# Performance work log

Measured on AMD Instinct MI355X. Metric: run time of the kernel, lower is better.

The kernel has to match this reference:

```python
import jax, jax.numpy as jnp
import numpy as np

jax.config.update("jax_enable_x64", True)  # original solves the quartic in double/complex128

MU = 1.33
SCALE = 1.0
N_RAYS = 2_000_000


def _solve2nd(a, b, c):
    # roots of a x^2 + b x + c, complex128
    D = (b * b - 4 * a * c).astype(jnp.complex128)
    s = jnp.sqrt(D)
    return (-b + s) / (2 * a), (-b - s) / (2 * a)


def _solve3rd(a, b, c, d):
    # Cardano closed form, returns [N,3] complex128
    A0 = d / a
    A1 = c / a
    A2 = b / a
    p = A1 - A2 * A2 / 3
    q = A0 - A1 * A2 / 3 + A2 * A2 * A2 * 2 / 27
    D = (q / 2) ** 2 + (p / 3) ** 3 + 1e-12
    r = jnp.sqrt(D.astype(jnp.complex128))
    o = complex(-0.5, np.sqrt(3) / 2)
    L = jnp.power(-q / 2 + r, 1.0 / 3.0)
    R = jnp.power(-q / 2 - r, 1.0 / 3.0)
    x0 = L + R - A2 / 3
    x1 = o * o * L + o * R - A2 / 3
    x2 = o * L + o * o * R - A2 / 3
    return jnp.stack([x0, x1, x2], axis=-1)


def _solve4th(coefs):
    # Ferrari via resolvent cubic; coefs [N,5] float64 -> roots [N,4] complex128
    a, b, c, d, e = (coefs[..., i] for i in range(5))
    A0 = e / a
    A1 = d / a
    A2 = c / a
    A3 = b / a
    p = A2 - 6 * A3 * A3 / 16
    q = A1 - A2 * A3 / 2 + 8 * (A3 / 4) ** 3
    r = A0 - A1 * A3 / 4 + A2 * A3 * A3 / 16 - 3 * (A3 / 4) ** 4
    u = _solve3rd(jnp.ones_like(p), 2 * p, p * p - 4 * r, -q * q)  # [N,3] complex
    cost = jnp.where(u.real < 0, 1e6, jnp.abs(u.imag))
    idx = jnp.argmin(cost, axis=1)
    t = jnp.clip(jnp.take_along_axis(u.real, idx[:, None], axis=1)[:, 0], 1e-6, None)
    st = jnp.sqrt(t)
    y00, y01 = _solve2nd(jnp.ones_like(t), st, (p + t) / 2 - st * q / (2 * t))
    y10, y11 = _solve2nd(jnp.ones_like(t), -st, (p + t) / 2 + st * q / (2 * t))
    return jnp.stack([y00 - A3 / 4, y01 - A3 / 4, y10 - A3 / 4, y11 - A3 / 4], axis=-1)


def _forward_projection(pos3d, n, d_eff, mu):
    nvec = jnp.concatenate([n, jnp.ones((1,), pos3d.dtype)])
    normal = -(nvec / jnp.linalg.norm(nvec))[None, :]          # [1,3]
    por = jnp.cross(normal, pos3d)                              # [N,3]
    por = por / jnp.linalg.norm(por, axis=-1, keepdims=True)
    z1 = -normal                                                # [1,3]
    z2 = jnp.cross(por, jnp.broadcast_to(z1, por.shape))        # [N,3]
    v = jnp.sum(pos3d * z1, axis=-1)                            # [N]
    u = jnp.sum(pos3d * z2, axis=-1)                            # [N]
    c2 = -2 * u * (mu - 1) * (mu + 1)
    c1 = jnp.ones_like(c2) * ((mu - 1) * (mu + 1))
    c3 = d_eff * d_eff * mu * mu - d_eff * d_eff + 2 * d_eff * v + mu * mu * u * u - u * u - v * v
    c4 = -2 * d_eff * d_eff * mu * mu * u
    c5 = d_eff * d_eff * mu * mu * u * u
    coefs = jnp.stack([c1, c2, c3, c4, c5], axis=-1).astype(jnp.float64)
    x0 = _solve4th(coefs).astype(jnp.complex64).T               # [4,N]
    xx = x0.real.astype(jnp.float32)                            # [4,N]
    n2 = jnp.array([0.0, -1.0], jnp.float32)
    vi = jnp.stack([xx, jnp.ones_like(xx) * d_eff], axis=-1)    # [4,N,2]
    bb = jnp.sum(vi * n2, axis=-1)
    bbb = jnp.sum(vi * vi, axis=-1)
    b = (-bb - jnp.sqrt(bb * bb - (1 - mu * mu) * bbb)) / mu
    vr = (1.0 / mu) * vi + b[..., None] * n2                    # refracted 2D dirs
    vrd = jnp.stack([u, v], axis=-1)[None] - vi                 # [4,N,2]
    error = jnp.abs(vrd[..., 0] * vr[..., 1] - vrd[..., 1] * vr[..., 0])
    error = jnp.where(jnp.abs(x0.imag) > 0.001, jnp.inf, error)
    best = jnp.take_along_axis(xx, jnp.argmin(error, axis=0)[None, :], axis=0)[0]
    return best[:, None] * z2 + d_eff * z1                      # [N,3]


def setup_inputs() -> dict:
    key = jax.random.key(0)
    k1, k2, k3 = jax.random.split(key, 3)
    pos3d = jax.random.normal(k1, (N_RAYS, 3), dtype=jnp.float32)
    # put points at positive depth so refraction geometry is sensible
    pos3d = pos3d.at[:, 2].set(jnp.abs(pos3d[:, 2]) + 0.5)
    n = jax.random.normal(k2, (2,), dtype=jnp.float32) * 0.02   # near-flat interface normal xy
    d = jax.random.uniform(k3, (), dtype=jnp.float32) * 0.5 + 0.2  # scalar depth param
    return {"pos3d": pos3d, "n": n, "d": d}


def reference(pos3d, n, d):
    mu = jnp.float32(MU)
    d_eff = jax.nn.relu(d) / SCALE + 0.001
    return _forward_projection(pos3d, n, d_eff, mu)
```

## Files before the change

kernel.cpp:

```cpp
#include <hip/hip_runtime.h>
#include <math.h>


__device__ __forceinline__ float fast_rcp(float x) { return __builtin_amdgcn_rcpf(x); }
__device__ __forceinline__ float fast_rsq(float x) { return __builtin_amdgcn_rsqf(x); }

__device__ __forceinline__ void cbrt_cw(double x, double& c, double& w) {
    float xf = (float)x;
    float wf = __builtin_amdgcn_exp2f(__builtin_amdgcn_logf(xf) * (-1.0f / 3.0f));
    double wd = (double)wf;
    wd = wd * (4.0 - x * ((wd * wd) * wd)) * (1.0 / 3.0);
    bool tiny = (x < 1e-30);
    w = tiny ? 0.0 : wd;
    c = tiny ? 0.0 : x * (wd * wd);
}

__global__ __launch_bounds__(256) void refract_kernel(
    const float* __restrict__ pos,
    const float* __restrict__ nrm,
    const float* __restrict__ dpt,
    float* __restrict__ out,
    int N)
{
    int i = blockIdx.x * blockDim.x + threadIdx.x;
    if (i >= N) return;

    const float mu = 1.33f;
    float n0 = nrm[0], n1 = nrm[1];
    float d_eff = fmaxf(dpt[0], 0.0f) + 0.001f;

    float nn = sqrtf(n0 * n0 + n1 * n1 + 1.0f);
    float z1x = n0 / nn, z1y = n1 / nn, z1z = 1.0f / nn;

    float px = pos[3 * i + 0], py = pos[3 * i + 1], pz = pos[3 * i + 2];

    float cux = z1y * pz - z1z * py;
    float cuy = z1z * px - z1x * pz;
    float cuz = z1x * py - z1y * px;
    float pn = sqrtf(cux * cux + cuy * cuy + cuz * cuz);
    float u = -pn;
    float ipn = fast_rcp(pn);
    float z2x = (z1y * cuz - z1z * cuy) * ipn;
    float z2y = (z1z * cux - z1x * cuz) * ipn;
    float z2z = (z1x * cuy - z1y * cux) * ipn;

    float v = px * z1x + py * z1y + pz * z1z;

    float c3f = d_eff * d_eff * mu * mu - d_eff * d_eff + 2.0f * d_eff * v
              + mu * mu * u * u - u * u - v * v;

    const double invc1 = 1.0 / (double)((1.33f - 1.0f) * (1.33f + 1.0f));
    const double mu2d = (double)(1.33f) * (double)(1.33f);
    double dm = (double)d_eff;
    double km = -2.0 * dm * dm * mu2d * invc1;

    double ud = (double)u;
    double G  = (double)c3f * invc1;
    double U  = ud * ud;
    double p  = fma(-1.5, U, G);
    double q  = ud * ((G - U) + km);
    double r  = 0.25 * U * fma(-0.75, U, G);
    double p2 = p * p;
    double q2 = q * q;
    double pr = p * r;
    double p3 = p2 * p;
    double mql = fma(p3, 1.0 / 27.0, fma(pr, -4.0 / 3.0, 0.5 * q2));
    double pc3 = fma(p2, -1.0 / 9.0, (-4.0 / 3.0) * r);
    double Dc  = fma(pc3 * pc3, pc3, fma(mql, mql, 1e-12));
    double sh  = p * (2.0 / 3.0);
    double p2d = p + p;

    double t;

    if (Dc < 0.0) {
        float R2f = (float)(-pc3);
        float Rf  = sqrtf(R2f);
        float cphi = (float)mql * fast_rcp(R2f * Rf);
        cphi = fminf(fmaxf(cphi, -1.0f), 1.0f);
        float T = 0.5f + sqrtf((1.0f + cphi) * (1.0f / 6.0f));
        #pragma unroll
        for (int k = 0; k < 3; ++k) {
            float g  = fmaf(fmaf(4.0f * T, T, -3.0f), T, -cphi);
            float gp = fmaf(12.0f * T, T, -3.0f);
            T -= g * fast_rcp(gp + 1e-12f);
        }
        t = (double)(2.0f * Rf * T) - sh;

        double B1n = fma(-4.0, r, p2);
        double f   = ((t + p2d) * t + B1n) * t - q2;
        double fp  = fma(3.0 * t + p2d, t, (t * p2d + B1n));
        double fpp = 6.0 * t + 2.0 * p2d;
        double den = fp * fp - 0.5 * f * fpp;
        double inv = (double)fast_rcp((float)den);
        inv = inv * (2.0 - den * inv);
        double dt  = (f * fp) * inv;
        if (isfinite(dt) && fabs(dt) < 0.1 * fabs(t) + 1e-2) t -= dt;
    } else {
        double rcr;
        if (Dc < 1e-36) {
            rcr = 0.0;
        } else {
            double z = (double)fast_rsq((float)Dc);
            z = z * (1.5 - 0.5 * Dc * (z * z));
            rcr = Dc * z;
        }
        double aa = mql + rcr;
        double bb = mql - rcr;
        bool na = (aa < 0.0), nb = (bb < 0.0);

        double absa = fabs(aa), absb = fabs(bb);
        bool aBig = (absa >= absb);
        double big = aBig ? absa : absb;
        double cbig, wbig;
        cbrt_cw(big, cbig, wbig);
        double csml = fabs(pc3) * wbig;
        double ca = aBig ? cbig : csml;
        double cb = aBig ? csml : cbig;

        if (!na && !nb) {
            double s = ca + cb;
            double u0r = s - sh;
            t = (u0r >= 0.0) ? u0r : fma(-0.5, s, -sh);
        } else {
            const double CI = 0.8660254037844386;
            double Lre = na ? 0.5 * ca : ca;
            double Lim = na ? CI * ca  : 0.0;
            double Rre = nb ? 0.5 * cb : cb;
            double Rim = nb ? CI * cb  : 0.0;

            double u0r = (Lre + Rre) - sh;
            double u0i =  Lim + Rim;
            double u1r = (-0.5 * Lre + CI * Lim) + (-0.5 * Rre - CI * Rim) - sh;
            double u1i = (-0.5 * Lim - CI * Lre) + (-0.5 * Rim + CI * Rre);
            double u2r = (-0.5 * Lre - CI * Lim) + (-0.5 * Rre + CI * Rim) - sh;
            double u2i = (-0.5 * Lim + CI * Lre) + (-0.5 * Rim - CI * Rre);

            double c0 = (u0r < 0.0) ? 1e6 : fabs(u0i);
            double c1 = (u1r < 0.0) ? 1e6 : fabs(u1i);
            double c2 = (u2r < 0.0) ? 1e6 : fabs(u2i);
            double cbest = c0; t = u0r;
            if (c1 < cbest) { cbest = c1; t = u1r; }
            if (c2 < cbest) { t = u2r; }
        }
    }

    t = fmax(t, 1e-6);
    double rs = (double)fast_rsq((float)t);
    rs = rs * (1.5 - 0.5 * t * (rs * rs));
    double st = t * rs;
    double tp = t + p2d;
    double wq = 2.0 * (q * rs);
    double D1 = wq - tp;
    double D2 = -wq - tp;

    float s1r = 0.0f, s1i = 0.0f, s2r = 0.0f, s2i = 0.0f;
    if (D1 >= 0.0) s1r = sqrtf((float)D1); else s1i = sqrtf((float)(-D1));
    if (D2 >= 0.0) s2r = sqrtf((float)D2); else s2i = sqrtf((float)(-D2));
    bool im1 = (s1i * 0.5f > 0.001f);
    bool im2 = (s2i * 0.5f > 0.001f);

    float stf = (float)st;
    float uh  = 0.5f * u;
    float xr0 = (-stf + s1r) * 0.5f + uh;
    float xr1 = (-stf - s1r) * 0.5f + uh;
    float xr2 = ( stf + s2r) * 0.5f + uh;
    float xr3 = ( stf - s2r) * 0.5f + uh;

    float mm2 = mu * mu - 1.0f;
    float mude2 = mu * mu * d_eff * d_eff;
    float vd = v - d_eff;
    float g0 = fmaf(mm2, xr0 * xr0, mude2);
    float g1 = fmaf(mm2, xr1 * xr1, mude2);
    float g2 = fmaf(mm2, xr2 * xr2, mude2);
    float g3 = fmaf(mm2, xr3 * xr3, mude2);
    float e0 = im1 ? INFINITY : fabsf((u - xr0) * sqrtf(g0) - vd * xr0);
    float e1 = im1 ? INFINITY : fabsf((u - xr1) * sqrtf(g1) - vd * xr1);
    float e2 = im2 ? INFINITY : fabsf((u - xr2) * sqrtf(g2) - vd * xr2);
    float e3 = im2 ? INFINITY : fabsf((u - xr3) * sqrtf(g3) - vd * xr3);

    float best = xr0; float eb = e0;
    if (e1 < eb) { eb = e1; best = xr1; }
    if (e2 < eb) { eb = e2; best = xr2; }
    if (e3 < eb) { eb = e3; best = xr3; }

    out[3 * i + 0] = best * z2x + d_eff * z1x;
    out[3 * i + 1] = best * z2y + d_eff * z1y;
    out[3 * i + 2] = best * z2z + d_eff * z1z;
}

extern "C" void kernel_launch(void* const* d_in, const int* in_sizes, int n_in,
                              void* d_out, int out_size, void* d_ws, size_t ws_size,
                              hipStream_t stream) {
    const float* pos = (const float*)d_in[0];
    const float* nrm = (const float*)d_in[1];
    const float* dpt = (const float*)d_in[2];
    float* out = (float*)d_out;
    int N = in_sizes[0] / 3;
    int block = 256;
    int grid = (N + block - 1) / block;
    refract_kernel<<<grid, block, 0, stream>>>(pos, nrm, dpt, out, N);
}
```

Before: 29.00 us.

## Run cubic root branch in fp32 with flagged fp64 rescue path

The non-trigonometric Cardano branch now runs in single precision, using an fp32 cube root and fp32 complex root selection, instead of double precision. A set of conditioning checks marks lanes where fp32 may pick the wrong root: near-zero discriminants, near-tied selection costs, and near-zero quadratic discriminants. Those lanes recompute the full original fp64 path in a noinline rescue function. This aims to cut the slow fp64 work per ray, at the cost of extra flag arithmetic, a divergent rescue call and possible accuracy misses the heuristics do not catch.

New measurement: 40.16 us. +38.5%, slower.

```diff
diff --git a/kernel.cpp b/kernel.cpp
--- a/kernel.cpp
+++ b/kernel.cpp
@@ -5,7 +5,14 @@
 __device__ __forceinline__ float fast_rcp(float x) { return __builtin_amdgcn_rcpf(x); }
 __device__ __forceinline__ float fast_rsq(float x) { return __builtin_amdgcn_rsqf(x); }
 
-__device__ __forceinline__ void cbrt_cw(double x, double& c, double& w) {
+__device__ __forceinline__ float cbrtf_pos(float x) {
+    float w = __builtin_amdgcn_exp2f(__builtin_amdgcn_logf(x) * (-1.0f / 3.0f));
+    w = w * (4.0f - x * ((w * w) * w)) * (1.0f / 3.0f);
+    float c = x * (w * w);
+    return (x < 1e-30f) ? 0.0f : c;
+}
+
+__device__ __forceinline__ void cbrt_cw64(double x, double& c, double& w) {
     float xf = (float)x;
     float wf = __builtin_amdgcn_exp2f(__builtin_amdgcn_logf(xf) * (-1.0f / 3.0f));
     double wd = (double)wf;
@@ -13,6 +20,113 @@
     bool tiny = (x < 1e-30);
     w = tiny ? 0.0 : wd;
     c = tiny ? 0.0 : x * (wd * wd);
+}
+
+__device__ __attribute__((noinline)) float rescue_fp64(
+    double q, double q2, double B1n, double mql, double pc3,
+    double Dc, double sh, double p2d,
+    float u, float mm2, float mude2, float vd)
+{
+    double t;
+    if (Dc < 0.0) {
+        float R2f = (float)(-pc3);
+        float Rf  = sqrtf(R2f);
+        float cphi = (float)mql * fast_rcp(R2f * Rf);
+        cphi = fminf(fmaxf(cphi, -1.0f), 1.0f);
+        float T = 0.5f + sqrtf((1.0f + cphi) * (1.0f / 6.0f));
+        #pragma unroll
+        for (int k = 0; k < 3; ++k) {
+            float g  = fmaf(fmaf(4.0f * T, T, -3.0f), T, -cphi);
+            float gp = fmaf(12.0f * T, T, -3.0f);
+            T -= g * fast_rcp(gp + 1e-12f);
+        }
+        t = (double)(2.0f * Rf * T) - sh;
+        double f   = ((t + p2d) * t + B1n) * t - q2;
+        double fp_ = fma(3.0 * t + p2d, t, (t * p2d + B1n));
+        double fpp = 6.0 * t + 2.0 * p2d;
+        double den = fp_ * fp_ - 0.5 * f * fpp;
+        double inv = (double)fast_rcp((float)den);
+        inv = inv * (2.0 - den * inv);
+        double dt  = (f * fp_) * inv;
+        if (isfinite(dt) && fabs(dt) < 0.1 * fabs(t) + 1e-2) t -= dt;
+    } else {
+        double rcr;
+        if (Dc < 1e-36) rcr = 0.0;
+        else {
+            double z = (double)fast_rsq((float)Dc);
+            z = z * (1.5 - 0.5 * Dc * (z * z));
+            rcr = Dc * z;
+        }
+        double aa = mql + rcr, bb = mql - rcr;
+        bool na = (aa < 0.0), nb = (bb < 0.0);
+        double absa = fabs(aa), absb = fabs(bb);
+        bool aBig = (absa >= absb);
+        double big = aBig ? absa : absb;
+        double cbig, wbig;
+        cbrt_cw64(big, cbig, wbig);
+        double csml = fabs(pc3) * wbig;
+        double ca = aBig ? cbig : csml;
+        double cb = aBig ? csml : cbig;
+        if (!na && !nb) {
+            double s = ca + cb;
+            double u0r = s - sh;
+            t = (u0r >= 0.0) ? u0r : fma(-0.5, s, -sh);
+        } else {
+            const double CI = 0.8660254037844386;
+            double Lre = na ? 0.5 * ca : ca;
+            double Lim = na ? CI * ca  : 0.0;
+            double Rre = nb ? 0.5 * cb : cb;
+            double Rim = nb ? CI * cb  : 0.0;
+            double u0r = (Lre + Rre) - sh;
+            double u0i =  Lim + Rim;
+            double u1r = (-0.5 * Lre + CI * Lim) + (-0.5 * Rre - CI * Rim) - sh;
+            double u1i = (-0.5 * Lim - CI * Lre) + (-0.5 * Rim + CI * Rre);
+            double u2r = (-0.5 * Lre - CI * Lim) + (-0.5 * Rre + CI * Rim) - sh;
+            double u2i = (-0.5 * Lim + CI * Lre) + (-0.5 * Rim - CI * Rre);
+            double c0 = (u0r < 0.0) ? 1e6 : fabs(u0i);
+            double c1 = (u1r < 0.0) ? 1e6 : fabs(u1i);
+            double c2 = (u2r < 0.0) ? 1e6 : fabs(u2i);
+            double cbest = c0; t = u0r;
+            if (c1 < cbest) { cbest = c1; t = u1r; }
+            if (c2 < cbest) { t = u2r; }
+        }
+    }
+
+    t = fmax(t, 1e-6);
+    double rs = (double)fast_rsq((float)t);
+    rs = rs * (1.5 - 0.5 * t * (rs * rs));
+    double wq = 2.0 * (q * rs);
+    double tp = t + p2d;
+    double D1 = wq - tp;
+    double D2 = -wq - tp;
+
+    float s1r = 0.0f, s1i = 0.0f, s2r = 0.0f, s2i = 0.0f;
+    if (D1 >= 0.0) s1r = sqrtf((float)D1); else s1i = sqrtf((float)(-D1));
+    if (D2 >= 0.0) s2r = sqrtf((float)D2); else s2i = sqrtf((float)(-D2));
+    bool im1 = (s1i * 0.5f > 0.001f);
+    bool im2 = (s2i * 0.5f > 0.001f);
+
+    float stf = (float)(t * rs);
+    float uh  = 0.5f * u;
+    float xr0 = (-stf + s1r) * 0.5f + uh;
+    float xr1 = (-stf - s1r) * 0.5f + uh;
+    float xr2 = ( stf + s2r) * 0.5f + uh;
+    float xr3 = ( stf - s2r) * 0.5f + uh;
+
+    float g0 = fmaf(mm2, xr0 * xr0, mude2);
+    float g1 = fmaf(mm2, xr1 * xr1, mude2);
+    float g2 = fmaf(mm2, xr2 * xr2, mude2);
+    float g3 = fmaf(mm2, xr3 * xr3, mude2);
+    float e0 = im1 ? INFINITY : fabsf((u - xr0) * sqrtf(g0) - vd * xr0);
+    float e1 = im1 ? INFINITY : fabsf((u - xr1) * sqrtf(g1) - vd * xr1);
+    float e2 = im2 ? INFINITY : fabsf((u - xr2) * sqrtf(g2) - vd * xr2);
+    float e3 = im2 ? INFINITY : fabsf((u - xr3) * sqrtf(g3) - vd * xr3);
+
+    float best = xr0; float eb = e0;
+    if (e1 < eb) { eb = e1; best = xr1; }
+    if (e2 < eb) { eb = e2; best = xr2; }
+    if (e3 < eb) { eb = e3; best = xr3; }
+    return best;
 }
 
 __global__ __launch_bounds__(256) void refract_kernel(
@@ -66,16 +180,26 @@
     double p3 = p2 * p;
     double mql = fma(p3, 1.0 / 27.0, fma(pr, -4.0 / 3.0, 0.5 * q2));
     double pc3 = fma(p2, -1.0 / 9.0, (-4.0 / 3.0) * r);
-    double Dc  = fma(pc3 * pc3, pc3, fma(mql, mql, 1e-12));
+    double pc33 = (pc3 * pc3) * pc3;
+    double mql2 = mql * mql;
+    double Dc   = pc33 + (mql2 + 1e-12);
+    double scDc = fabs(pc33) + mql2 + 1e-12;
     double sh  = p * (2.0 / 3.0);
     double p2d = p + p;
+    double B1n = fma(-4.0, r, p2);
+
+    bool flag = fabs(Dc) < 1e-12 * scDc;
+
+    float mqlf = (float)mql;
+    float shf  = (float)sh;
 
     double t;
+    bool polish = false;
 
     if (Dc < 0.0) {
         float R2f = (float)(-pc3);
         float Rf  = sqrtf(R2f);
-        float cphi = (float)mql * fast_rcp(R2f * Rf);
+        float cphi = mqlf * fast_rcp(R2f * Rf);
         cphi = fminf(fmaxf(cphi, -1.0f), 1.0f);
         float T = 0.5f + sqrtf((1.0f + cphi) * (1.0f / 6.0f));
         #pragma unroll
@@ -85,81 +209,87 @@
             T -= g * fast_rcp(gp + 1e-12f);
         }
         t = (double)(2.0f * Rf * T) - sh;
-
-        double B1n = fma(-4.0, r, p2);
+        polish = true;
+    } else {
+        float rcrf = sqrtf((float)Dc);
+        float aaf = mqlf + rcrf;
+        float bbf = mqlf - rcrf;
+        float abscale = fabsf(mqlf) + rcrf + 1e-20f;
+        flag = flag || (fabsf(aaf) < 2e-5f * abscale)
+                    || (fabsf(bbf) < 2e-5f * abscale);
+        bool na = (aaf < 0.0f), nb = (bbf < 0.0f);
+        float caf = cbrtf_pos(fabsf(aaf));
+        float cbf = cbrtf_pos(fabsf(bbf));
+
+        if (!na && !nb) {
+            float s = caf + cbf;
+            float u0rf = s - shf;
+            flag = flag || (fabsf(u0rf) < 3e-6f * (s + fabsf(shf) + 1e-20f));
+            if (u0rf >= 0.0f) { t = (double)u0rf; polish = true; }
+            else              { t = (double)fmaf(-0.5f, s, -shf); }
+        } else {
+            const float CI = 0.8660254f;
+            float Lre = na ? 0.5f * caf : caf;
+            float Lim = na ? CI * caf   : 0.0f;
+            float Rre = nb ? 0.5f * cbf : cbf;
+            float Rim = nb ? CI * cbf   : 0.0f;
+            float u0r = (Lre + Rre) - shf;
+            float u0i =  Lim + Rim;
+            float u1r = (-0.5f * Lre + CI * Lim) + (-0.5f * Rre - CI * Rim) - shf;
+            float u1i = (-0.5f * Lim - CI * Lre) + (-0.5f * Rim + CI * Rre);
+            float u2r = (-0.5f * Lre - CI * Lim) + (-0.5f * Rre + CI * Rim) - shf;
+            float u2i = (-0.5f * Lim + CI * Lre) + (-0.5f * Rim - CI * Rre);
+
+            float jscale = caf + cbf + fabsf(shf) + 1e-20f;
+            flag = flag || (fabsf(u0r) < 1e-5f * jscale)
+                        || (fabsf(u1r) < 1e-5f * jscale)
+                        || (fabsf(u2r) < 1e-5f * jscale);
+
+            float c0 = (u0r < 0.0f) ? 1e6f : fabsf(u0i);
+            float c1 = (u1r < 0.0f) ? 1e6f : fabsf(u1i);
+            float c2 = (u2r < 0.0f) ? 1e6f : fabsf(u2i);
+            float cbest = c0, tsel = u0r, csec;
+            if (c1 < cbest) { csec = cbest; cbest = c1; tsel = u1r; }
+            else            { csec = c1; }
+            if (c2 < cbest) { csec = cbest; cbest = c2; tsel = u2r; }
+            else            { csec = fminf(csec, c2); }
+            flag = flag || ((csec - cbest) < 1e-4f * (cbest + 1e-3f));
+            t = (double)tsel;
+        }
+    }
+
+    if (polish) {
         double f   = ((t + p2d) * t + B1n) * t - q2;
-        double fp  = fma(3.0 * t + p2d, t, (t * p2d + B1n));
+        double fp_ = fma(3.0 * t + p2d, t, (t * p2d + B1n));
         double fpp = 6.0 * t + 2.0 * p2d;
-        double den = fp * fp - 0.5 * f * fpp;
+        double den = fp_ * fp_ - 0.5 * f * fpp;
         double inv = (double)fast_rcp((float)den);
         inv = inv * (2.0 - den * inv);
-        double dt  = (f * fp) * inv;
+        double dt  = (f * fp_) * inv;
         if (isfinite(dt) && fabs(dt) < 0.1 * fabs(t) + 1e-2) t -= dt;
-    } else {
-        double rcr;
-        if (Dc < 1e-36) {
-            rcr = 0.0;
-        } else {
-            double z = (double)fast_rsq((float)Dc);
-            z = z * (1.5 - 0.5 * Dc * (z * z));
-            rcr = Dc * z;
-        }
-        double aa = mql + rcr;
-        double bb = mql - rcr;
-        bool na = (aa < 0.0), nb = (bb < 0.0);
-
-        double absa = fabs(aa), absb = fabs(bb);
-        bool aBig = (absa >= absb);
-        double big = aBig ? absa : absb;
-        double cbig, wbig;
-        cbrt_cw(big, cbig, wbig);
-        double csml = fabs(pc3) * wbig;
-        double ca = aBig ? cbig : csml;
-        double cb = aBig ? csml : cbig;
-
-        if (!na && !nb) {
-            double s = ca + cb;
-            double u0r = s - sh;
-            t = (u0r >= 0.0) ? u0r : fma(-0.5, s, -sh);
-        } else {
-            const double CI = 0.8660254037844386;
-            double Lre = na ? 0.5 * ca : ca;
-            double Lim = na ? CI * ca  : 0.0;
-            double Rre = nb ? 0.5 * cb : cb;
-            double Rim = nb ? CI * cb  : 0.0;
-
-            double u0r = (Lre + Rre) - sh;
-            double u0i =  Lim + Rim;
-            double u1r = (-0.5 * Lre + CI * Lim) + (-0.5 * Rre - CI * Rim) - sh;
-            double u1i = (-0.5 * Lim - CI * Lre) + (-0.5 * Rim + CI * Rre);
-            double u2r = (-0.5 * Lre - CI * Lim) + (-0.5 * Rre + CI * Rim) - sh;
-            double u2i = (-0.5 * Lim + CI * Lre) + (-0.5 * Rim - CI * Rre);
-
-            double c0 = (u0r < 0.0) ? 1e6 : fabs(u0i);
-            double c1 = (u1r < 0.0) ? 1e6 : fabs(u1i);
-            double c2 = (u2r < 0.0) ? 1e6 : fabs(u2i);
-            double cbest = c0; t = u0r;
-            if (c1 < cbest) { cbest = c1; t = u1r; }
-            if (c2 < cbest) { t = u2r; }
-        }
+        else flag = true;
     }
 
     t = fmax(t, 1e-6);
     double rs = (double)fast_rsq((float)t);
     rs = rs * (1.5 - 0.5 * t * (rs * rs));
-    double st = t * rs;
+    double wq = 2.0 * (q * rs);
     double tp = t + p2d;
-    double wq = 2.0 * (q * rs);
     double D1 = wq - tp;
     double D2 = -wq - tp;
 
+    float D1f = (float)D1, D2f = (float)D2;
+    float MDf = fabsf((float)wq) + fabsf((float)tp);
+    float wwin = (polish ? 1e-7f : 1e-4f * (1.0f + MDf)) + 5e-6f;
+    flag = flag || (fabsf(D1f) < wwin) || (fabsf(D2f) < wwin);
+
     float s1r = 0.0f, s1i = 0.0f, s2r = 0.0f, s2i = 0.0f;
-    if (D1 >= 0.0) s1r = sqrtf((float)D1); else s1i = sqrtf((float)(-D1));
-    if (D2 >= 0.0) s2r = sqrtf((float)D2); else s2i = sqrtf((float)(-D2));
+    if (D1 >= 0.0) s1r = sqrtf(D1f); else s1i = sqrtf(-D1f);
+    if (D2 >= 0.0) s2r = sqrtf(D2f); else s2i = sqrtf(-D2f);
     bool im1 = (s1i * 0.5f > 0.001f);
     bool im2 = (s2i * 0.5f > 0.001f);
 
-    float stf = (float)st;
+    float stf = (float)(t * rs);
     float uh  = 0.5f * u;
     float xr0 = (-stf + s1r) * 0.5f + uh;
     float xr1 = (-stf - s1r) * 0.5f + uh;
@@ -178,10 +308,22 @@
     float e2 = im2 ? INFINITY : fabsf((u - xr2) * sqrtf(g2) - vd * xr2);
     float e3 = im2 ? INFINITY : fabsf((u - xr3) * sqrtf(g3) - vd * xr3);
 
-    float best = xr0; float eb = e0;
-    if (e1 < eb) { eb = e1; best = xr1; }
-    if (e2 < eb) { eb = e2; best = xr2; }
-    if (e3 < eb) { eb = e3; best = xr3; }
+    float eb = e0, xb = xr0, eb2, xb2;
+    if (e1 < eb) { eb2 = eb; xb2 = xb; eb = e1; xb = xr1; }
+    else         { eb2 = e1; xb2 = xr1; }
+    if (e2 < eb) { eb2 = eb; xb2 = xb; eb = e2; xb = xr2; }
+    else if (e2 < eb2) { eb2 = e2; xb2 = xr2; }
+    if (e3 < eb) { eb2 = eb; xb2 = xb; eb = e3; xb = xr3; }
+    else if (e3 < eb2) { eb2 = e3; xb2 = xr3; }
+
+    float margin = (polish ? 3e-5f : 3e-4f) * (1.0f + eb) + 1e-6f;
+    if (((eb2 - eb) < margin) && (fabsf(xb2 - xb) > 3e-2f)) flag = true;
+
+    float best = xb;
+    if (__builtin_expect(flag, 0)) {
+        best = rescue_fp64(q, q2, B1n, mql, pc3, Dc, sh, p2d,
+                           u, mm2, mude2, vd);
+    }
 
     out[3 * i + 0] = best * z2x + d_eff * z1x;
     out[3 * i + 1] = best * z2y + d_eff * z1y;
```
